# Performance work log

Hardware: AMD Instinct MI355X
Metric: run time of the kernel (lower is better)

Reference implementation:

```python
import jax, jax.numpy as jnp
import numpy as np

N_NODES = 50000
N_EDGES = 800000
DIM = 64
N_HEADS = 4


def setup_inputs() -> dict:
    key = jax.random.key(0)
    ks = jax.random.split(key, 7)
    x = jax.random.normal(ks[0], (N_NODES, DIM), dtype=jnp.float32)
    Wq = jax.random.normal(ks[1], (DIM, DIM), dtype=jnp.float32) / np.sqrt(DIM)
    Wk = jax.random.normal(ks[2], (DIM, DIM), dtype=jnp.float32) / np.sqrt(DIM)
    Wv = jax.random.normal(ks[3], (DIM, DIM), dtype=jnp.float32) / np.sqrt(DIM)
    Wo = jax.random.normal(ks[4], (DIM, DIM), dtype=jnp.float32) / np.sqrt(DIM)
    src = jax.random.randint(ks[5], (N_EDGES,), 0, N_NODES, dtype=jnp.int32)
    dst = jax.random.randint(ks[6], (N_EDGES,), 0, N_NODES, dtype=jnp.int32)
    return {"x": x, "Wq": Wq, "Wk": Wk, "Wv": Wv, "Wo": Wo, "src": src, "dst": dst}


def _scatter_softmax(scores, dst, n_nodes):
    # scores: [E, H]; per-destination-node softmax over incoming edges.
    m = jax.ops.segment_max(scores, dst, num_segments=n_nodes)  # [N, H]
    m = jnp.maximum(m, jnp.float32(-1e9))  # mirror the -1e9 init of the torch code
    ex = jnp.exp(scores - m[dst])  # [E, H]
    denom = jax.ops.segment_sum(ex, dst, num_segments=n_nodes)  # [N, H]
    return ex / (denom[dst] + 1e-9)


def reference(x, Wq, Wk, Wv, Wo, src, dst):
    N, D = x.shape
    H = N_HEADS
    Dh = D // H
    q = (x @ Wq).reshape(N, H, Dh)
    k = (x @ Wk).reshape(N, H, Dh)
    v = (x @ Wv).reshape(N, H, Dh)
    # per-edge attention logits: [E, H]
    scores = jnp.einsum("ehd,ehd->eh", q[dst], k[src]) / jnp.sqrt(jnp.float32(Dh))
    alpha = _scatter_softmax(scores, dst, N)  # [E, H]
    # weighted aggregation of source values onto destination nodes
    agg = jax.ops.segment_sum(alpha[:, :, None] * v[src], dst, num_segments=N)  # [N, H, Dh]
    return agg.reshape(N, D) @ Wo
```

## Files before the change

kernel.cpp:

```cpp
#include <hip/hip_runtime.h>
#include <math.h>

#define HEADS 4
#define DH 16
#define D 64
#define MAXDEG 64
#define NXCD 8

typedef unsigned short ushort_t;
typedef unsigned int uint_t;

__device__ __forceinline__ float bf2f(ushort_t u) {
    return __uint_as_float(((uint_t)u) << 16);
}
__device__ __forceinline__ ushort_t f2bf(float f) {
    uint_t u = __float_as_uint(f);
    u = (u + 0x7FFFu + ((u >> 16) & 1u)) >> 16;
    return (ushort_t)u;
}

__global__ __launch_bounds__(256) void qkv_kernel(const float* __restrict__ x,
                                                  const float* __restrict__ Wq,
                                                  const float* __restrict__ Wk,
                                                  const float* __restrict__ Wv,
                                                  float* __restrict__ q,
                                                  ushort_t* __restrict__ kbf,
                                                  ushort_t* __restrict__ vbf,
                                                  int* __restrict__ cursor,
                                                  int N) {
    __shared__ float wq[D][D];
    __shared__ float wk[D][D];
    __shared__ float wv[D][D];
    __shared__ float xs[16][D];

    int tid = threadIdx.x;
    for (int i = tid; i < D * D; i += 256) {
        wq[i >> 6][i & 63] = Wq[i];
        wk[i >> 6][i & 63] = Wk[i];
        wv[i >> 6][i & 63] = Wv[i];
    }

    int c = tid & 63;
    int g = tid >> 6;
    int row = tid >> 4;
    int col4 = tid & 15;

    int ntiles = (N + 15) >> 4;
    for (int tile = blockIdx.x; tile < ntiles; tile += gridDim.x) {
        int n0t = tile * 16;
        __syncthreads();
        float4 xv = make_float4(0.f, 0.f, 0.f, 0.f);
        if (n0t + row < N) xv = *(const float4*)(x + (size_t)(n0t + row) * D + col4 * 4);
        *(float4*)&xs[row][col4 * 4] = xv;
        __syncthreads();

        float aq0=0,aq1=0,aq2=0,aq3=0, ak0=0,ak1=0,ak2=0,ak3=0, av0=0,av1=0,av2=0,av3=0;
#pragma unroll 8
        for (int d = 0; d < D; ++d) {
            float wqv = wq[d][c], wkv = wk[d][c], wvv = wv[d][c];
            float x0 = xs[g*4+0][d], x1 = xs[g*4+1][d], x2 = xs[g*4+2][d], x3 = xs[g*4+3][d];
            aq0 += x0*wqv; ak0 += x0*wkv; av0 += x0*wvv;
            aq1 += x1*wqv; ak1 += x1*wkv; av1 += x1*wvv;
            aq2 += x2*wqv; ak2 += x2*wkv; av2 += x2*wvv;
            aq3 += x3*wqv; ak3 += x3*wkv; av3 += x3*wvv;
        }
        int nb = n0t + g * 4;
        if (nb+0 < N) { q[(size_t)(nb+0)*D+c]=aq0; kbf[(size_t)(nb+0)*D+c]=f2bf(ak0); vbf[(size_t)(nb+0)*D+c]=f2bf(av0); }
        if (nb+1 < N) { q[(size_t)(nb+1)*D+c]=aq1; kbf[(size_t)(nb+1)*D+c]=f2bf(ak1); vbf[(size_t)(nb+1)*D+c]=f2bf(av1); }
        if (nb+2 < N) { q[(size_t)(nb+2)*D+c]=aq2; kbf[(size_t)(nb+2)*D+c]=f2bf(ak2); vbf[(size_t)(nb+2)*D+c]=f2bf(av2); }
        if (nb+3 < N) { q[(size_t)(nb+3)*D+c]=aq3; kbf[(size_t)(nb+3)*D+c]=f2bf(ak3); vbf[(size_t)(nb+3)*D+c]=f2bf(av3); }
    }

    for (int i = blockIdx.x * 256 + tid; i < N; i += gridDim.x * 256) cursor[i] = 0;
}

__global__ __launch_bounds__(256) void scatter_kernel(const int* __restrict__ src,
                                                      const int* __restrict__ dst,
                                                      int* __restrict__ cursor,
                                                      ushort_t* __restrict__ csr,
                                                      int E, int N) {
    int p      = blockIdx.x & (NXCD - 1);
    int chunk  = blockIdx.x >> 3;
    int nchunk = gridDim.x >> 3;
    int lo = (int)((long long)N * p / NXCD);
    int hi = (int)((long long)N * (p + 1) / NXCD);
    int e0 = (int)((long long)E * chunk / nchunk);
    int e1 = (int)((long long)E * (chunk + 1) / nchunk);

    for (int e = e0 + threadIdx.x; e < e1; e += 256) {
        int d = dst[e];
        if (d >= lo && d < hi) {
            int pos = atomicAdd(&cursor[d], 1);
            if (pos < MAXDEG) csr[(size_t)d * MAXDEG + pos] = (ushort_t)src[e];
        }
    }
}

__global__ __launch_bounds__(256) void attn_kernel(const float* __restrict__ q,
                                                   const ushort_t* __restrict__ kbf,
                                                   const ushort_t* __restrict__ vbf,
                                                   const ushort_t* __restrict__ csr,
                                                   const int* __restrict__ cursor,
                                                   float* __restrict__ agg,
                                                   float* __restrict__ denom,
                                                   int N) {
    int lane = threadIdx.x & 63;
    int wave = threadIdx.x >> 6;
    int node = blockIdx.x * 4 + wave;
    if (node >= N) return;

    int hp  = lane & 3;
    int el  = lane >> 2;
    int hd  = (lane & 31) >> 3;
    int par = lane >> 5;
    int dp2 = 2 * (lane & 31);

    int cnt = cursor[node]; if (cnt > MAXDEG) cnt = MAXDEG;
    const ushort_t* row = csr + (size_t)node * MAXDEG;

    float qr[16];
    {
        const float4* qp = (const float4*)(q + (size_t)node * D + hp * DH);
        *(float4*)&qr[0]  = qp[0];
        *(float4*)&qr[4]  = qp[1];
        *(float4*)&qr[8]  = qp[2];
        *(float4*)&qr[12] = qp[3];
    }

    int s0=0, s1=0, s2=0, s3=0;
    float sc0=-1e30f, sc1=-1e30f, sc2=-1e30f, sc3=-1e30f;

#define PH1SB(sb, sv, scv)                                                      \
    if ((sb) * 16 < cnt) {                                                      \
        int eidx = (sb) * 16 + el;                                              \
        if (eidx < cnt) sv = row[eidx];                                         \
        const uint4* kp = (const uint4*)(kbf + (size_t)sv * D + hp * DH);       \
        uint4 ka = kp[0], kb = kp[1];                                           \
        float dot =                                                             \
          __uint_as_float(ka.x << 16)          * qr[0]                          \
        + __uint_as_float(ka.x & 0xFFFF0000u)  * qr[1]                          \
        + __uint_as_float(ka.y << 16)          * qr[2]                          \
        + __uint_as_float(ka.y & 0xFFFF0000u)  * qr[3]                          \
        + __uint_as_float(ka.z << 16)          * qr[4]                          \
        + __uint_as_float(ka.z & 0xFFFF0000u)  * qr[5]                          \
        + __uint_as_float(ka.w << 16)          * qr[6]                          \
        + __uint_as_float(ka.w & 0xFFFF0000u)  * qr[7]                          \
        + __uint_as_float(kb.x << 16)          * qr[8]                          \
        + __uint_as_float(kb.x & 0xFFFF0000u)  * qr[9]                          \
        + __uint_as_float(kb.y << 16)          * qr[10]                         \
        + __uint_as_float(kb.y & 0xFFFF0000u)  * qr[11]                         \
        + __uint_as_float(kb.z << 16)          * qr[12]                         \
        + __uint_as_float(kb.z & 0xFFFF0000u)  * qr[13]                         \
        + __uint_as_float(kb.w << 16)          * qr[14]                         \
        + __uint_as_float(kb.w & 0xFFFF0000u)  * qr[15];                        \
        scv = (eidx < cnt) ? dot * 0.25f : -1e30f;                              \
    }
    PH1SB(0, s0, sc0)
    PH1SB(1, s1, sc1)
    PH1SB(2, s2, sc2)
    PH1SB(3, s3, sc3)
#undef PH1SB

    float mloc = fmaxf(fmaxf(sc0, sc1), fmaxf(sc2, sc3));
    mloc = fmaxf(mloc, __shfl_xor(mloc, 4, 64));
    mloc = fmaxf(mloc, __shfl_xor(mloc, 8, 64));
    mloc = fmaxf(mloc, __shfl_xor(mloc, 16, 64));
    mloc = fmaxf(mloc, __shfl_xor(mloc, 32, 64));
    mloc = fmaxf(mloc, -1e9f);

    float pv0 = __expf(sc0 - mloc);
    float pv1 = __expf(sc1 - mloc);
    float pv2 = __expf(sc2 - mloc);
    float pv3 = __expf(sc3 - mloc);
    float ls = (pv0 + pv1) + (pv2 + pv3);
    ls += __shfl_xor(ls, 4, 64);
    ls += __shfl_xor(ls, 8, 64);
    ls += __shfl_xor(ls, 16, 64);
    ls += __shfl_xor(ls, 32, 64);

    if (lane < HEADS) denom[(size_t)node * HEADS + lane] = ls;

    float2 a0 = {0.f, 0.f}, a1 = {0.f, 0.f};
#define PH3SB(sb, sv, pvv)                                                      \
    if ((sb) * 16 < cnt) {                                                      \
        int lim = cnt - (sb) * 16; if (lim > 16) lim = 16;                      \
        for (int e2 = 0; e2 < lim; e2 += 4) {                                   \
            int L0 = 4 * (e2 + par);                                            \
            int ss0 = __shfl(sv, L0, 64);                                       \
            float p0 = __shfl(pvv, L0 + hd, 64);                                \
            uint_t w0 = *(const uint_t*)(vbf + (size_t)ss0 * D + dp2);          \
            a0.x += p0 * __uint_as_float(w0 << 16);                             \
            a0.y += p0 * __uint_as_float(w0 & 0xFFFF0000u);                     \
            int L1 = 4 * (e2 + 2 + par);                                        \
            int ss1 = __shfl(sv, L1, 64);                                       \
            float p1 = __shfl(pvv, L1 + hd, 64);                                \
            uint_t w1 = *(const uint_t*)(vbf + (size_t)ss1 * D + dp2);          \
            a1.x += p1 * __uint_as_float(w1 << 16);                             \
            a1.y += p1 * __uint_as_float(w1 & 0xFFFF0000u);                     \
        }                                                                       \
    }
    PH3SB(0, s0, pv0)
    PH3SB(1, s1, pv1)
    PH3SB(2, s2, pv2)
    PH3SB(3, s3, pv3)
#undef PH3SB

    float ax = a0.x + a1.x, ay = a0.y + a1.y;
    ax += __shfl_xor(ax, 32, 64);
    ay += __shfl_xor(ay, 32, 64);
    if (lane < 32) {
        *(float2*)(agg + (size_t)node * D + dp2) = make_float2(ax, ay);
    }
}

__global__ __launch_bounds__(256) void out_kernel(const float* __restrict__ agg,
                                                  const float* __restrict__ denom,
                                                  const float* __restrict__ Wo,
                                                  float* __restrict__ out, int N) {
    __shared__ float wo[D][D];
    __shared__ float xs[16][D];

    int tid = threadIdx.x;
    for (int i = tid; i < D * D; i += 256) wo[i >> 6][i & 63] = Wo[i];

    int c = tid & 63;
    int g = tid >> 6;
    int row = tid >> 4;
    int col4 = tid & 15;

    int ntiles = (N + 15) >> 4;
    for (int tile = blockIdx.x; tile < ntiles; tile += gridDim.x) {
        int n0 = tile * 16;
        __syncthreads();
        float4 av = make_float4(0.f, 0.f, 0.f, 0.f);
        if (n0 + row < N) {
            av = *(const float4*)(agg + (size_t)(n0 + row) * D + col4 * 4);
            float inv = 1.f / (denom[(size_t)(n0 + row) * HEADS + (col4 >> 2)] + 1e-9f);
            av.x *= inv; av.y *= inv; av.z *= inv; av.w *= inv;
        }
        *(float4*)&xs[row][col4 * 4] = av;
        __syncthreads();

        float a0 = 0.f, a1 = 0.f, a2 = 0.f, a3 = 0.f;
#pragma unroll 8
        for (int d = 0; d < D; ++d) {
            float w = wo[d][c];
            a0 += xs[g*4+0][d] * w;
            a1 += xs[g*4+1][d] * w;
            a2 += xs[g*4+2][d] * w;
            a3 += xs[g*4+3][d] * w;
        }
        int nb = n0 + g * 4;
        if (nb+0 < N) out[(size_t)(nb+0)*D+c] = a0;
        if (nb+1 < N) out[(size_t)(nb+1)*D+c] = a1;
        if (nb+2 < N) out[(size_t)(nb+2)*D+c] = a2;
        if (nb+3 < N) out[(size_t)(nb+3)*D+c] = a3;
    }
}

extern "C" void kernel_launch(void* const* d_in, const int* in_sizes, int n_in,
                              void* d_out, int out_size, void* d_ws, size_t ws_size,
                              hipStream_t stream) {
    const float* x  = (const float*)d_in[0];
    const float* Wq = (const float*)d_in[1];
    const float* Wk = (const float*)d_in[2];
    const float* Wv = (const float*)d_in[3];
    const float* Wo = (const float*)d_in[4];
    const int* src  = (const int*)d_in[5];
    const int* dst  = (const int*)d_in[6];
    float* out = (float*)d_out;

    int N = in_sizes[0] / D;
    int E = in_sizes[5];

    char* ws = (char*)d_ws;
    float* q      = (float*)ws;     ws += (size_t)N * D * 4;
    float* agg    = (float*)ws;     ws += (size_t)N * D * 4;
    ushort_t* kbf = (ushort_t*)ws;  ws += (size_t)N * D * 2;
    ushort_t* vbf = (ushort_t*)ws;  ws += (size_t)N * D * 2;
    float* denom  = (float*)ws;     ws += (size_t)N * HEADS * 4;
    int* cursor   = (int*)ws;       ws += (size_t)N * 4;
    ushort_t* csr = (ushort_t*)ws;  ws += (size_t)N * MAXDEG * 2;

    int nTiles16 = (N + 15) / 16;
    int gemmGrid = nTiles16 < 2048 ? nTiles16 : 2048;
    int attnGrid = (N + 3) / 4;

    qkv_kernel<<<gemmGrid, 256, 0, stream>>>(x, Wq, Wk, Wv, q, kbf, vbf, cursor, N);
    scatter_kernel<<<2048, 256, 0, stream>>>(src, dst, cursor, csr, E, N);
    attn_kernel<<<attnGrid, 256, 0, stream>>>(q, kbf, vbf, csr, cursor, agg, denom, N);
    out_kernel<<<gemmGrid, 256, 0, stream>>>(agg, denom, Wo, out, N);
}
```

Measured before the change: 129.9 us.

## Store q and normalized agg in bf16, fold softmax normalization into attention

Q and the aggregated output are now stored as bf16 instead of fp32, which halves those intermediate buffers' traffic. The softmax denominator is applied inside the attention kernel, so the separate denom buffer and its reads in the output GEMM go away. The QKV and output GEMMs also transpose their weights into padded shared memory and use float4 LDS reads. The trade-off is extra rounding error from bf16 q and agg.

```diff
diff --git a/kernel.cpp b/kernel.cpp
--- a/kernel.cpp
+++ b/kernel.cpp
@@ -18,26 +18,32 @@
     u = (u + 0x7FFFu + ((u >> 16) & 1u)) >> 16;
     return (ushort_t)u;
 }
+__device__ __forceinline__ float bflo(uint_t u) { return __uint_as_float(u << 16); }
+__device__ __forceinline__ float bfhi(uint_t u) { return __uint_as_float(u & 0xFFFF0000u); }
+__device__ __forceinline__ uint_t pack2(float a, float b) {
+    return (uint_t)f2bf(a) | ((uint_t)f2bf(b) << 16);
+}
 
 __global__ __launch_bounds__(256) void qkv_kernel(const float* __restrict__ x,
                                                   const float* __restrict__ Wq,
                                                   const float* __restrict__ Wk,
                                                   const float* __restrict__ Wv,
-                                                  float* __restrict__ q,
+                                                  ushort_t* __restrict__ qbf,
                                                   ushort_t* __restrict__ kbf,
                                                   ushort_t* __restrict__ vbf,
                                                   int* __restrict__ cursor,
                                                   int N) {
-    __shared__ float wq[D][D];
-    __shared__ float wk[D][D];
-    __shared__ float wv[D][D];
-    __shared__ float xs[16][D];
+    __shared__ float wt[3][D][68];
+    __shared__ float xs[16][68];
 
     int tid = threadIdx.x;
-    for (int i = tid; i < D * D; i += 256) {
-        wq[i >> 6][i & 63] = Wq[i];
-        wk[i >> 6][i & 63] = Wk[i];
-        wv[i >> 6][i & 63] = Wv[i];
+    for (int i = tid; i < 3 * D * D; i += 256) {
+        int m = i >> 12;
+        int r = i & 4095;
+        int d = r & 63;
+        int c = r >> 6;
+        const float* W = (m == 0) ? Wq : (m == 1) ? Wk : Wv;
+        wt[m][c][d] = W[d * D + c];
     }
 
     int c = tid & 63;
@@ -55,20 +61,33 @@
         __syncthreads();
 
         float aq0=0,aq1=0,aq2=0,aq3=0, ak0=0,ak1=0,ak2=0,ak3=0, av0=0,av1=0,av2=0,av3=0;
-#pragma unroll 8
-        for (int d = 0; d < D; ++d) {
-            float wqv = wq[d][c], wkv = wk[d][c], wvv = wv[d][c];
-            float x0 = xs[g*4+0][d], x1 = xs[g*4+1][d], x2 = xs[g*4+2][d], x3 = xs[g*4+3][d];
-            aq0 += x0*wqv; ak0 += x0*wkv; av0 += x0*wvv;
-            aq1 += x1*wqv; ak1 += x1*wkv; av1 += x1*wvv;
-            aq2 += x2*wqv; ak2 += x2*wkv; av2 += x2*wvv;
-            aq3 += x3*wqv; ak3 += x3*wkv; av3 += x3*wvv;
+#pragma unroll
+        for (int d4 = 0; d4 < 16; ++d4) {
+            float4 wq4 = *(const float4*)&wt[0][c][d4 * 4];
+            float4 wk4 = *(const float4*)&wt[1][c][d4 * 4];
+            float4 wv4 = *(const float4*)&wt[2][c][d4 * 4];
+            float4 x0 = *(const float4*)&xs[g * 4 + 0][d4 * 4];
+            float4 x1 = *(const float4*)&xs[g * 4 + 1][d4 * 4];
+            float4 x2 = *(const float4*)&xs[g * 4 + 2][d4 * 4];
+            float4 x3 = *(const float4*)&xs[g * 4 + 3][d4 * 4];
+            aq0 += x0.x*wq4.x + x0.y*wq4.y + x0.z*wq4.z + x0.w*wq4.w;
+            ak0 += x0.x*wk4.x + x0.y*wk4.y + x0.z*wk4.z + x0.w*wk4.w;
+            av0 += x0.x*wv4.x + x0.y*wv4.y + x0.z*wv4.z + x0.w*wv4.w;
+            aq1 += x1.x*wq4.x + x1.y*wq4.y + x1.z*wq4.z + x1.w*wq4.w;
+            ak1 += x1.x*wk4.x + x1.y*wk4.y + x1.z*wk4.z + x1.w*wk4.w;
+            av1 += x1.x*wv4.x + x1.y*wv4.y + x1.z*wv4.z + x1.w*wv4.w;
+            aq2 += x2.x*wq4.x + x2.y*wq4.y + x2.z*wq4.z + x2.w*wq4.w;
+            ak2 += x2.x*wk4.x + x2.y*wk4.y + x2.z*wk4.z + x2.w*wk4.w;
+            av2 += x2.x*wv4.x + x2.y*wv4.y + x2.z*wv4.z + x2.w*wv4.w;
+            aq3 += x3.x*wq4.x + x3.y*wq4.y + x3.z*wq4.z + x3.w*wq4.w;
+            ak3 += x3.x*wk4.x + x3.y*wk4.y + x3.z*wk4.z + x3.w*wk4.w;
+            av3 += x3.x*wv4.x + x3.y*wv4.y + x3.z*wv4.z + x3.w*wv4.w;
         }
         int nb = n0t + g * 4;
-        if (nb+0 < N) { q[(size_t)(nb+0)*D+c]=aq0; kbf[(size_t)(nb+0)*D+c]=f2bf(ak0); vbf[(size_t)(nb+0)*D+c]=f2bf(av0); }
-        if (nb+1 < N) { q[(size_t)(nb+1)*D+c]=aq1; kbf[(size_t)(nb+1)*D+c]=f2bf(ak1); vbf[(size_t)(nb+1)*D+c]=f2bf(av1); }
-        if (nb+2 < N) { q[(size_t)(nb+2)*D+c]=aq2; kbf[(size_t)(nb+2)*D+c]=f2bf(ak2); vbf[(size_t)(nb+2)*D+c]=f2bf(av2); }
-        if (nb+3 < N) { q[(size_t)(nb+3)*D+c]=aq3; kbf[(size_t)(nb+3)*D+c]=f2bf(ak3); vbf[(size_t)(nb+3)*D+c]=f2bf(av3); }
+        if (nb+0 < N) { qbf[(size_t)(nb+0)*D+c]=f2bf(aq0); kbf[(size_t)(nb+0)*D+c]=f2bf(ak0); vbf[(size_t)(nb+0)*D+c]=f2bf(av0); }
+        if (nb+1 < N) { qbf[(size_t)(nb+1)*D+c]=f2bf(aq1); kbf[(size_t)(nb+1)*D+c]=f2bf(ak1); vbf[(size_t)(nb+1)*D+c]=f2bf(av1); }
+        if (nb+2 < N) { qbf[(size_t)(nb+2)*D+c]=f2bf(aq2); kbf[(size_t)(nb+2)*D+c]=f2bf(ak2); vbf[(size_t)(nb+2)*D+c]=f2bf(av2); }
+        if (nb+3 < N) { qbf[(size_t)(nb+3)*D+c]=f2bf(aq3); kbf[(size_t)(nb+3)*D+c]=f2bf(ak3); vbf[(size_t)(nb+3)*D+c]=f2bf(av3); }
     }
 
     for (int i = blockIdx.x * 256 + tid; i < N; i += gridDim.x * 256) cursor[i] = 0;
@@ -96,13 +115,12 @@
     }
 }
 
-__global__ __launch_bounds__(256) void attn_kernel(const float* __restrict__ q,
+__global__ __launch_bounds__(256) void attn_kernel(const ushort_t* __restrict__ qbf,
                                                    const ushort_t* __restrict__ kbf,
                                                    const ushort_t* __restrict__ vbf,
                                                    const ushort_t* __restrict__ csr,
                                                    const int* __restrict__ cursor,
-                                                   float* __restrict__ agg,
-                                                   float* __restrict__ denom,
+                                                   ushort_t* __restrict__ aggbf,
                                                    int N) {
     int lane = threadIdx.x & 63;
     int wave = threadIdx.x >> 6;
@@ -120,11 +138,12 @@
 
     float qr[16];
     {
-        const float4* qp = (const float4*)(q + (size_t)node * D + hp * DH);
-        *(float4*)&qr[0]  = qp[0];
-        *(float4*)&qr[4]  = qp[1];
-        *(float4*)&qr[8]  = qp[2];
-        *(float4*)&qr[12] = qp[3];
+        const uint4* qp = (const uint4*)(qbf + (size_t)node * D + hp * DH);
+        uint4 qa = qp[0], qb = qp[1];
+        qr[0]=bflo(qa.x);  qr[1]=bfhi(qa.x);  qr[2]=bflo(qa.y);  qr[3]=bfhi(qa.y);
+        qr[4]=bflo(qa.z);  qr[5]=bfhi(qa.z);  qr[6]=bflo(qa.w);  qr[7]=bfhi(qa.w);
+        qr[8]=bflo(qb.x);  qr[9]=bfhi(qb.x);  qr[10]=bflo(qb.y); qr[11]=bfhi(qb.y);
+        qr[12]=bflo(qb.z); qr[13]=bfhi(qb.z); qr[14]=bflo(qb.w); qr[15]=bfhi(qb.w);
     }
 
     int s0=0, s1=0, s2=0, s3=0;
@@ -137,22 +156,14 @@
         const uint4* kp = (const uint4*)(kbf + (size_t)sv * D + hp * DH);       \
         uint4 ka = kp[0], kb = kp[1];                                           \
         float dot =                                                             \
-          __uint_as_float(ka.x << 16)          * qr[0]                          \
-        + __uint_as_float(ka.x & 0xFFFF0000u)  * qr[1]                          \
-        + __uint_as_float(ka.y << 16)          * qr[2]                          \
-        + __uint_as_float(ka.y & 0xFFFF0000u)  * qr[3]                          \
-        + __uint_as_float(ka.z << 16)          * qr[4]                          \
-        + __uint_as_float(ka.z & 0xFFFF0000u)  * qr[5]                          \
-        + __uint_as_float(ka.w << 16)          * qr[6]                          \
-        + __uint_as_float(ka.w & 0xFFFF0000u)  * qr[7]                          \
-        + __uint_as_float(kb.x << 16)          * qr[8]                          \
-        + __uint_as_float(kb.x & 0xFFFF0000u)  * qr[9]                          \
-        + __uint_as_float(kb.y << 16)          * qr[10]                         \
-        + __uint_as_float(kb.y & 0xFFFF0000u)  * qr[11]                         \
-        + __uint_as_float(kb.z << 16)          * qr[12]                         \
-        + __uint_as_float(kb.z & 0xFFFF0000u)  * qr[13]                         \
-        + __uint_as_float(kb.w << 16)          * qr[14]                         \
-        + __uint_as_float(kb.w & 0xFFFF0000u)  * qr[15];                        \
+          bflo(ka.x)*qr[0]  + bfhi(ka.x)*qr[1]                                  \
+        + bflo(ka.y)*qr[2]  + bfhi(ka.y)*qr[3]                                  \
+        + bflo(ka.z)*qr[4]  + bfhi(ka.z)*qr[5]                                  \
+        + bflo(ka.w)*qr[6]  + bfhi(ka.w)*qr[7]                                  \
+        + bflo(kb.x)*qr[8]  + bfhi(kb.x)*qr[9]                                  \
+        + bflo(kb.y)*qr[10] + bfhi(kb.y)*qr[11]                                 \
+        + bflo(kb.z)*qr[12] + bfhi(kb.z)*qr[13]                                 \
+        + bflo(kb.w)*qr[14] + bfhi(kb.w)*qr[15];                                \
         scv = (eidx < cnt) ? dot * 0.25f : -1e30f;                              \
     }
     PH1SB(0, s0, sc0)
@@ -178,7 +189,7 @@
     ls += __shfl_xor(ls, 16, 64);
     ls += __shfl_xor(ls, 32, 64);
 
-    if (lane < HEADS) denom[(size_t)node * HEADS + lane] = ls;
+    float inv = 1.f / (__shfl(ls, hd, 64) + 1e-9f);
 
     float2 a0 = {0.f, 0.f}, a1 = {0.f, 0.f};
 #define PH3SB(sb, sv, pvv)                                                      \
@@ -189,14 +200,14 @@
             int ss0 = __shfl(sv, L0, 64);                                       \
             float p0 = __shfl(pvv, L0 + hd, 64);                                \
             uint_t w0 = *(const uint_t*)(vbf + (size_t)ss0 * D + dp2);          \
-            a0.x += p0 * __uint_as_float(w0 << 16);                             \
-            a0.y += p0 * __uint_as_float(w0 & 0xFFFF0000u);                     \
+            a0.x += p0 * bflo(w0);                                              \
+            a0.y += p0 * bfhi(w0);                                              \
             int L1 = 4 * (e2 + 2 + par);                                        \
             int ss1 = __shfl(sv, L1, 64);                                       \
             float p1 = __shfl(pvv, L1 + hd, 64);                                \
             uint_t w1 = *(const uint_t*)(vbf + (size_t)ss1 * D + dp2);          \
-            a1.x += p1 * __uint_as_float(w1 << 16);                             \
-            a1.y += p1 * __uint_as_float(w1 & 0xFFFF0000u);                     \
+            a1.x += p1 * bflo(w1);                                              \
+            a1.y += p1 * bfhi(w1);                                              \
         }                                                                       \
     }
     PH3SB(0, s0, pv0)
@@ -209,19 +220,22 @@
     ax += __shfl_xor(ax, 32, 64);
     ay += __shfl_xor(ay, 32, 64);
     if (lane < 32) {
-        *(float2*)(agg + (size_t)node * D + dp2) = make_float2(ax, ay);
-    }
-}
-
-__global__ __launch_bounds__(256) void out_kernel(const float* __restrict__ agg,
-                                                  const float* __restrict__ denom,
+        *(uint_t*)(aggbf + (size_t)node * D + dp2) = pack2(ax * inv, ay * inv);
+    }
+}
+
+__global__ __launch_bounds__(256) void out_kernel(const ushort_t* __restrict__ aggbf,
                                                   const float* __restrict__ Wo,
                                                   float* __restrict__ out, int N) {
-    __shared__ float wo[D][D];
-    __shared__ float xs[16][D];
+    __shared__ float wt[D][68];
+    __shared__ float xs[16][68];
 
     int tid = threadIdx.x;
-    for (int i = tid; i < D * D; i += 256) wo[i >> 6][i & 63] = Wo[i];
+    for (int i = tid; i < D * D; i += 256) {
+        int d = i & 63;
+        int c = i >> 6;
+        wt[c][d] = Wo[d * D + c];
+    }
 
     int c = tid & 63;
     int g = tid >> 6;
@@ -232,23 +246,26 @@
     for (int tile = blockIdx.x; tile < ntiles; tile += gridDim.x) {
         int n0 = tile * 16;
         __syncthreads();
-        float4 av = make_float4(0.f, 0.f, 0.f, 0.f);
-        if (n0 + row < N) {
-            av = *(const float4*)(agg + (size_t)(n0 + row) * D + col4 * 4);
-            float inv = 1.f / (denom[(size_t)(n0 + row) * HEADS + (col4 >> 2)] + 1e-9f);
-            av.x *= inv; av.y *= inv; av.z *= inv; av.w *= inv;
-        }
-        *(float4*)&xs[row][col4 * 4] = av;
+        uint2 av = make_uint2(0u, 0u);
+        if (n0 + row < N) av = *(const uint2*)(aggbf + (size_t)(n0 + row) * D + col4 * 4);
+        xs[row][col4 * 4 + 0] = bflo(av.x);
+        xs[row][col4 * 4 + 1] = bfhi(av.x);
+        xs[row][col4 * 4 + 2] = bflo(av.y);
+        xs[row][col4 * 4 + 3] = bfhi(av.y);
         __syncthreads();
 
         float a0 = 0.f, a1 = 0.f, a2 = 0.f, a3 = 0.f;
-#pragma unroll 8
-        for (int d = 0; d < D; ++d) {
-            float w = wo[d][c];
-            a0 += xs[g*4+0][d] * w;
-            a1 += xs[g*4+1][d] * w;
-            a2 += xs[g*4+2][d] * w;
-            a3 += xs[g*4+3][d] * w;
+#pragma unroll
+        for (int d4 = 0; d4 < 16; ++d4) {
+            float4 w4 = *(const float4*)&wt[c][d4 * 4];
+            float4 x0 = *(const float4*)&xs[g * 4 + 0][d4 * 4];
+            float4 x1 = *(const float4*)&xs[g * 4 + 1][d4 * 4];
+            float4 x2 = *(const float4*)&xs[g * 4 + 2][d4 * 4];
+            float4 x3 = *(const float4*)&xs[g * 4 + 3][d4 * 4];
+            a0 += x0.x*w4.x + x0.y*w4.y + x0.z*w4.z + x0.w*w4.w;
+            a1 += x1.x*w4.x + x1.y*w4.y + x1.z*w4.z + x1.w*w4.w;
+            a2 += x2.x*w4.x + x2.y*w4.y + x2.z*w4.z + x2.w*w4.w;
+            a3 += x3.x*w4.x + x3.y*w4.y + x3.z*w4.z + x3.w*w4.w;
         }
         int nb = n0 + g * 4;
         if (nb+0 < N) out[(size_t)(nb+0)*D+c] = a0;
@@ -274,20 +291,19 @@
     int E = in_sizes[5];
 
     char* ws = (char*)d_ws;
-    float* q      = (float*)ws;     ws += (size_t)N * D * 4;
-    float* agg    = (float*)ws;     ws += (size_t)N * D * 4;
-    ushort_t* kbf = (ushort_t*)ws;  ws += (size_t)N * D * 2;
-    ushort_t* vbf = (ushort_t*)ws;  ws += (size_t)N * D * 2;
-    float* denom  = (float*)ws;     ws += (size_t)N * HEADS * 4;
-    int* cursor   = (int*)ws;       ws += (size_t)N * 4;
-    ushort_t* csr = (ushort_t*)ws;  ws += (size_t)N * MAXDEG * 2;
+    ushort_t* qbf   = (ushort_t*)ws;  ws += (size_t)N * D * 2;
+    ushort_t* kbf   = (ushort_t*)ws;  ws += (size_t)N * D * 2;
+    ushort_t* vbf   = (ushort_t*)ws;  ws += (size_t)N * D * 2;
+    ushort_t* aggbf = (ushort_t*)ws;  ws += (size_t)N * D * 2;
+    int* cursor     = (int*)ws;       ws += (size_t)N * 4;
+    ushort_t* csr   = (ushort_t*)ws;  ws += (size_t)N * MAXDEG * 2;
 
     int nTiles16 = (N + 15) / 16;
     int gemmGrid = nTiles16 < 2048 ? nTiles16 : 2048;
     int attnGrid = (N + 3) / 4;
 
-    qkv_kernel<<<gemmGrid, 256, 0, stream>>>(x, Wq, Wk, Wv, q, kbf, vbf, cursor, N);
+    qkv_kernel<<<gemmGrid, 256, 0, stream>>>(x, Wq, Wk, Wv, qbf, kbf, vbf, cursor, N);
     scatter_kernel<<<2048, 256, 0, stream>>>(src, dst, cursor, csr, E, N);
-    attn_kernel<<<attnGrid, 256, 0, stream>>>(q, kbf, vbf, csr, cursor, agg, denom, N);
-    out_kernel<<<gemmGrid, 256, 0, stream>>>(agg, denom, Wo, out, N);
-}
+    attn_kernel<<<attnGrid, 256, 0, stream>>>(qbf, kbf, vbf, csr, cursor, aggbf, N);
+    out_kernel<<<gemmGrid, 256, 0, stream>>>(aggbf, Wo, out, N);
+}
```

Measured after the change: 222.6 us. +71.3%, slower.
